# Performance work log

Measured on AMD Instinct MI355X. Metric: run time of the kernel, lower is better.

## Reference

```python
import jax, jax.numpy as jnp
import numpy as np


def setup_inputs() -> dict:
    key = jax.random.key(0)
    k1, k2, k3 = jax.random.split(key, 3)
    B, C, H, W = 16, 256, 32, 32
    K, D = 8192, 256
    z = jax.random.normal(k1, (B, C, H, W), dtype=jnp.float32)
    # torch init: uniform(-1/K, 1/K); use small-scale values for realism
    embedding = jax.random.uniform(k2, (K, D), dtype=jnp.float32,
                                   minval=-1.0 / K, maxval=1.0 / K)
    proj_w = jax.random.normal(k3, (D, D), dtype=jnp.float32) * (1.0 / np.sqrt(D))
    return {"z": z, "embedding": embedding, "proj_w": proj_w}


def reference(z, embedding, proj_w):
    commitment_cost = 0.25
    B, C, H, W = z.shape
    # codebook = Linear(embedding) with no bias: emb @ W^T  -> [K, D]
    codebook = embedding @ proj_w.T
    zt = jnp.transpose(z, (0, 2, 3, 1))            # [B, H, W, C]
    zf = zt.reshape(-1, C)                          # [N, C], N = B*H*W
    # squared distances: ||z||^2 + ||e||^2 - 2 z.e  -> [N, K]
    d = (jnp.sum(zf * zf, axis=1, keepdims=True)
         + jnp.sum(codebook * codebook, axis=1)
         - 2.0 * jnp.einsum('nd,kd->nk', zf, codebook))
    min_encoding_indices = jnp.argmin(d, axis=1)    # [N]
    z_quantized = codebook[min_encoding_indices].reshape(zt.shape)  # [B,H,W,C]
    commitment_loss = commitment_cost * jnp.mean(
        (jax.lax.stop_gradient(z_quantized) - zt) ** 2)
    codebook_loss = jnp.mean((z_quantized - jax.lax.stop_gradient(zt)) ** 2)
    loss = commitment_loss + codebook_loss
    # straight-through estimator
    zq_st = zt + jax.lax.stop_gradient(z_quantized - zt)
    out = jnp.transpose(zq_st, (0, 3, 1, 2))        # [B, C, H, W]
    idx = min_encoding_indices.reshape(B, H, W)
    return out, loss, commitment_loss, codebook_loss, idx
```

## Files before the change

kernel.cpp:

```cpp
#include <hip/hip_runtime.h>
#include <cfloat>


constexpr int Dd = 256;
constexpr float INV_M = 1.0f / 4194304.0f;
constexpr float DLT = 1e-3f;

typedef unsigned short u16;
typedef unsigned int u32;
typedef __attribute__((ext_vector_type(8))) short short8;
typedef __attribute__((ext_vector_type(4))) float f32x4;

__device__ __forceinline__ unsigned monof(float f) {
  unsigned u = __float_as_uint(f);
  return (u & 0x80000000u) ? ~u : (u | 0x80000000u);
}
__device__ __forceinline__ float unmonof(unsigned p) {
  unsigned u = (p & 0x80000000u) ? (p & 0x7FFFFFFFu) : ~p;
  return __uint_as_float(u);
}
__device__ __forceinline__ u16 f2bf(float x) {
  unsigned u = __float_as_uint(x);
  u += 0x7FFFu + ((u >> 16) & 1u);
  return (u16)(u >> 16);
}

__global__ __launch_bounds__(256)
void k_codebook(const float* __restrict__ emb, const float* __restrict__ proj,
                float* __restrict__ cb, u16* __restrict__ ef) {
  __shared__ float et[64 * 65];
  __shared__ float pt[64 * 65];
  __shared__ __align__(16) u16 tileT[64 * 72];
  const int t = threadIdx.x;
  const int tx = t & 15, ty = t >> 4;
  const int kb = blockIdx.x * 64;
  const int db = blockIdx.y * 64;
  float acc[4][4];
#pragma unroll
  for (int u = 0; u < 4; ++u)
#pragma unroll
    for (int v = 0; v < 4; ++v) acc[u][v] = 0.f;

  const int jm = t & 15;
  const int q  = t >> 4;

  for (int jc = 0; jc < Dd; jc += 64) {
    __syncthreads();
#pragma unroll
    for (int i = 0; i < 4; ++i) {
      const int row = q + i * 16;
      const float4 e4 = *(const float4*)(emb  + (size_t)(kb + row) * Dd + jc + jm * 4);
      const float4 p4 = *(const float4*)(proj + (size_t)(db + row) * Dd + jc + jm * 4);
      et[(jm*4 + 0) * 65 + row] = e4.x;
      et[(jm*4 + 1) * 65 + row] = e4.y;
      et[(jm*4 + 2) * 65 + row] = e4.z;
      et[(jm*4 + 3) * 65 + row] = e4.w;
      pt[(jm*4 + 0) * 65 + row] = p4.x;
      pt[(jm*4 + 1) * 65 + row] = p4.y;
      pt[(jm*4 + 2) * 65 + row] = p4.z;
      pt[(jm*4 + 3) * 65 + row] = p4.w;
    }
    __syncthreads();
#pragma unroll 16
    for (int j = 0; j < 64; ++j) {
      float a[4], b[4];
#pragma unroll
      for (int u = 0; u < 4; ++u) a[u] = et[j*65 + ty*4 + u];
#pragma unroll
      for (int v = 0; v < 4; ++v) b[v] = pt[j*65 + tx*4 + v];
#pragma unroll
      for (int u = 0; u < 4; ++u)
#pragma unroll
        for (int v = 0; v < 4; ++v) acc[u][v] = fmaf(a[u], b[v], acc[u][v]);
    }
  }
#pragma unroll
  for (int u = 0; u < 4; ++u) {
    const int k = kb + ty*4 + u;
#pragma unroll
    for (int v = 0; v < 4; ++v) {
      const int d = db + tx*4 + v;
      const float val = acc[u][v];
      cb[(size_t)k * Dd + d] = val;
      tileT[(ty*4 + u) * 72 + tx*4 + v] = f2bf(val);
    }
  }
  __syncthreads();
  uint4* ef16 = (uint4*)ef;
#pragma unroll
  for (int w2 = 0; w2 < 2; ++w2) {
    const int uu = w2 * 256 + t;
    const int k16g = uu >> 7;
    const int d32g = (uu >> 6) & 1;
    const int ln   = uu & 63;
    const int klo  = k16g * 16 + (ln & 15);
    const int dlo  = d32g * 32 + (ln >> 4) * 8;
    ef16[((kb >> 4) + k16g) * 512 + ((db >> 5) + d32g) * 64 + ln] =
        *(const uint4*)&tileT[klo * 72 + dlo];
  }
}

__global__ __launch_bounds__(256)
void k_norms(const float* __restrict__ cb, float* __restrict__ norms) {
  const int k = blockIdx.x * 256 + threadIdx.x;
  const float* row = cb + (size_t)k * Dd;
  float s = 0.f;
  for (int d = 0; d < Dd; d += 4) {
    const float4 v = *(const float4*)(row + d);
    s = fmaf(v.x, v.x, s);
    s = fmaf(v.y, v.y, s);
    s = fmaf(v.z, v.z, s);
    s = fmaf(v.w, v.w, s);
  }
  norms[k] = s;
}

__global__ __launch_bounds__(256)
void k_prep_z(const float* __restrict__ z, u16* __restrict__ zf,
              float* __restrict__ znorm) {
  __shared__ float tile[256 * 33];
  const int t = threadIdx.x;
  const int blk = blockIdx.x;
  const int w = t & 31, rg = t >> 5;
  const size_t zbase = (size_t)(blk >> 5) * 262144 + (size_t)(blk & 31) * 32 + w;
#pragma unroll 8
  for (int i = 0; i < 32; ++i) {
    const int d = rg * 32 + i;
    tile[d * 33 + w] = z[zbase + (size_t)d * 1024];
  }
  __syncthreads();
  if (t < 32) {
    float s = 0.f;
    for (int d = 0; d < Dd; ++d) {
      const float v = tile[d * 33 + t];
      s = fmaf(v, v, s);
    }
    znorm[blk * 32 + t] = s;
  }
  const int ml16 = t & 15;
  const int seg  = (t >> 4) & 7;
  const int hi   = t >> 7;
  const int nl   = hi * 16 + ml16;
  uint4* zf16 = (uint4*)zf;
  const int ubase = ((blk * 2 + hi) * 8 + seg) * 64 + ml16;
#pragma unroll
  for (int j = 0; j < 4; ++j) {
    u16 hb[8];
#pragma unroll
    for (int e = 0; e < 8; ++e)
      hb[e] = f2bf(tile[(seg * 32 + j * 8 + e) * 33 + nl]);
    zf16[ubase + j * 16] = *(const uint4*)hb;
  }
}

template <bool EMIT>
__global__ __launch_bounds__(256, 2)
void k_scan(const u16* __restrict__ zf, const u16* __restrict__ ef,
            const float* __restrict__ norms, const float* __restrict__ znorm,
            u32* __restrict__ rowminG, const float* __restrict__ rowThr,
            u32* __restrict__ rowcnt, u16* __restrict__ slots) {
  const int t    = threadIdx.x;
  const int lane = t & 63;
  const int ml   = lane & 15;
  const int qd   = lane >> 4;
  const int wvu  = __builtin_amdgcn_readfirstlane(t >> 6);
  const int rowhalf = wvu & 1;
  const int colhalf = wvu >> 1;
  const int bid  = blockIdx.x;
  const int kb   = (bid & 7) * 1024;
  const int nb   = (bid >> 3) * 64;

  const uint4* za = (const uint4*)zf + (size_t)((nb >> 4) + rowhalf * 2) * 512 + lane;
  const uint4* eb = (const uint4*)ef + (size_t)((kb >> 4) + colhalf * 8) * 512 + lane;

  float zn[2][4], thr[2][4];
#pragma unroll
  for (int rt = 0; rt < 2; ++rt) {
    const int nr = nb + rowhalf * 32 + rt * 16 + qd * 4;
    const f32x4 z4 = *(const f32x4*)(znorm + nr);
#pragma unroll
    for (int r = 0; r < 4; ++r) zn[rt][r] = z4[r];
    if (EMIT) {
      const f32x4 t4 = *(const f32x4*)(rowThr + nr);
#pragma unroll
      for (int r = 0; r < 4; ++r) thr[rt][r] = t4[r];
    }
  }

  float mv[2][4];
#pragma unroll
  for (int rt = 0; rt < 2; ++rt)
#pragma unroll
    for (int r = 0; r < 4; ++r) mv[rt][r] = FLT_MAX;

  short8 A0[2], A1[2], B0[8], B1[8];
#pragma unroll
  for (int rt = 0; rt < 2; ++rt) A0[rt] = *(const short8*)(za + rt * 512);
#pragma unroll
  for (int ct = 0; ct < 8; ++ct) B0[ct] = *(const short8*)(eb + ct * 512);

#pragma unroll 1
  for (int kt = 0; kt < 4; ++kt) {
    float nk[8];
#pragma unroll
    for (int ct = 0; ct < 8; ++ct)
      nk[ct] = norms[kb + kt * 256 + colhalf * 128 + ct * 16 + ml];

    f32x4 acc[2][8];
#pragma unroll
    for (int rt = 0; rt < 2; ++rt)
#pragma unroll
      for (int ct = 0; ct < 8; ++ct) acc[rt][ct] = (f32x4)0.f;

#pragma unroll
    for (int dhp = 0; dhp < 8; ++dhp) {
      const int pn = kt * 8 + dhp + 1;
      if (pn < 32) {
        const int offa = (pn & 7) * 64;
        const int offb = (pn >> 3) * 8192 + (pn & 7) * 64;
        if (dhp & 1) {
#pragma unroll
          for (int rt = 0; rt < 2; ++rt)
            A0[rt] = *(const short8*)(za + rt * 512 + offa);
#pragma unroll
          for (int ct = 0; ct < 8; ++ct)
            B0[ct] = *(const short8*)(eb + ct * 512 + offb);
        } else {
#pragma unroll
          for (int rt = 0; rt < 2; ++rt)
            A1[rt] = *(const short8*)(za + rt * 512 + offa);
#pragma unroll
          for (int ct = 0; ct < 8; ++ct)
            B1[ct] = *(const short8*)(eb + ct * 512 + offb);
        }
      }
      if (dhp & 1) {
#pragma unroll
        for (int rt = 0; rt < 2; ++rt)
#pragma unroll
          for (int ct = 0; ct < 8; ++ct)
            acc[rt][ct] = __builtin_amdgcn_mfma_f32_16x16x32_bf16(
                A1[rt], B1[ct], acc[rt][ct], 0, 0, 0);
      } else {
#pragma unroll
        for (int rt = 0; rt < 2; ++rt)
#pragma unroll
          for (int ct = 0; ct < 8; ++ct)
            acc[rt][ct] = __builtin_amdgcn_mfma_f32_16x16x32_bf16(
                A0[rt], B0[ct], acc[rt][ct], 0, 0, 0);
      }
    }

#pragma unroll
    for (int ct = 0; ct < 8; ++ct) {
      const int k = kb + kt * 256 + colhalf * 128 + ct * 16 + ml;
      const float nkv = nk[ct];
#pragma unroll
      for (int rt = 0; rt < 2; ++rt)
#pragma unroll
        for (int r = 0; r < 4; ++r) {
          const float sc = (zn[rt][r] + nkv) - 2.0f * acc[rt][ct][r];
          if (!EMIT) {
            mv[rt][r] = fminf(mv[rt][r], sc);
          } else if (sc <= thr[rt][r]) {
            const int n = nb + rowhalf * 32 + rt * 16 + qd * 4 + r;
            const u32 pos = atomicAdd(&rowcnt[n], 1u);
            if (pos < 32u) slots[n * 32 + pos] = (u16)k;
          }
        }
    }
  }

  if (!EMIT) {
#pragma unroll
    for (int rt = 0; rt < 2; ++rt)
#pragma unroll
      for (int r = 0; r < 4; ++r) {
        float m = mv[rt][r];
#pragma unroll
        for (int s = 1; s < 16; s <<= 1) m = fminf(m, __shfl_xor(m, s, 64));
        if (ml == 0)
          atomicMin(&rowminG[nb + rowhalf * 32 + rt * 16 + qd * 4 + r], monof(m));
      }
  }
}

__global__ __launch_bounds__(256)
void k_thresh(const u32* __restrict__ rowminG, float* __restrict__ rowThr) {
  const int n = blockIdx.x * 256 + threadIdx.x;
  rowThr[n] = unmonof(rowminG[n]) + DLT;
}

__global__ __launch_bounds__(256)
void k_rescore(const float* __restrict__ z, const float* __restrict__ cb,
               const float* __restrict__ norms, const float* __restrict__ znorm,
               const u32* __restrict__ rowcnt, const u16* __restrict__ slots,
               unsigned long long* __restrict__ packed) {
  __shared__ float ztl[32 * 261];
  const int t = threadIdx.x;
  const int blk = blockIdx.x;
  const int w = t & 31, dg = t >> 5;
  const size_t zbase = (size_t)(blk >> 5) * 262144 + (size_t)(blk & 31) * 32;
#pragma unroll 8
  for (int i = 0; i < 32; ++i) {
    const int d = dg * 32 + i;
    ztl[w * 261 + d] = z[zbase + (size_t)d * 1024 + w];
  }
  __syncthreads();

  const int lane = t & 63;
  const int wv = t >> 6;
#pragma unroll 1
  for (int i = 0; i < 8; ++i) {
    const int rl = wv * 8 + i;
    const int n = blk * 32 + rl;
    const u32 cnt = min(rowcnt[n], 32u);
    const float znr = znorm[n];
    unsigned long long best = 0xFFFFFFFFFFFFFFFFull;
    for (u32 c = 0; c < cnt; ++c) {
      const int k = (int)slots[n * 32 + c];
      const float4 c4 = *(const float4*)(cb + (size_t)k * Dd + lane * 4);
      const float* zp = ztl + rl * 261 + lane * 4;
      float p = 0.f;
      p = fmaf(zp[0], c4.x, p);
      p = fmaf(zp[1], c4.y, p);
      p = fmaf(zp[2], c4.z, p);
      p = fmaf(zp[3], c4.w, p);
#pragma unroll
      for (int s = 1; s < 64; s <<= 1) p += __shfl_xor(p, s, 64);
      const float sc = (znr + norms[k]) - 2.0f * p;
      const unsigned long long pk =
          ((unsigned long long)monof(sc) << 32) | (unsigned)k;
      if (pk < best) best = pk;
    }
    if (lane == 0 && cnt > 0) packed[n] = best;
  }
}

__global__ __launch_bounds__(256)
void k_output(const float* __restrict__ z, const float* __restrict__ cb,
              const unsigned long long* __restrict__ packed,
              float* __restrict__ out, float* __restrict__ idxf,
              float* __restrict__ ssum) {
  __shared__ float zqT[256 * 33];
  __shared__ float part[4];
  const int t = threadIdx.x;
  const int blk = blockIdx.x;
  const int nbase = blk * 32;

  {
    const int nl = t >> 3, m = t & 7;
    const int idx = (int)(packed[nbase + nl] & 0xFFFFFFFFull);
    const float* row = cb + (size_t)idx * Dd;
#pragma unroll
    for (int i = 0; i < 8; ++i) {
      const int d0 = m * 4 + i * 32;
      const float4 v = *(const float4*)(row + d0);
      zqT[(d0 + 0) * 33 + nl] = v.x;
      zqT[(d0 + 1) * 33 + nl] = v.y;
      zqT[(d0 + 2) * 33 + nl] = v.z;
      zqT[(d0 + 3) * 33 + nl] = v.w;
    }
    if (t < 32)
      idxf[nbase + t] = (float)(unsigned)(packed[nbase + t] & 0xFFFFFFFFull);
  }
  __syncthreads();

  const int w = t & 31, cg = t >> 5;
  const size_t base = (size_t)(blk >> 5) * 262144 + (size_t)(blk & 31) * 32 + w;
  float local = 0.f;
#pragma unroll
  for (int cc = 0; cc < 32; ++cc) {
    const int c = cg * 32 + cc;
    const float q  = zqT[c * 33 + w];
    const float zv = z[base + (size_t)c * 1024];
    out[base + (size_t)c * 1024] = q;
    const float dd = q - zv;
    local = fmaf(dd, dd, local);
  }
  float v = local;
#pragma unroll
  for (int m = 1; m < 64; m <<= 1) v += __shfl_xor(v, m, 64);
  if ((t & 63) == 0) part[t >> 6] = v;
  __syncthreads();
  if (t == 0) atomicAdd(ssum, part[0] + part[1] + part[2] + part[3]);
}

__global__ void k_final(const float* __restrict__ ssum, float* __restrict__ scal) {
  const float m = *ssum * INV_M;
  scal[0] = 1.25f * m;
  scal[1] = 0.25f * m;
  scal[2] = m;
}

extern "C" void kernel_launch(void* const* d_in, const int* in_sizes, int n_in,
                              void* d_out, int out_size, void* d_ws, size_t ws_size,
                              hipStream_t stream) {
  const float* z    = (const float*)d_in[0];
  const float* emb  = (const float*)d_in[1];
  const float* proj = (const float*)d_in[2];

  float* out  = (float*)d_out;
  float* scal = out + 4194304;
  float* idxf = out + 4194307;

  float* cb    = (float*)d_ws;
  float* norms = cb + 2097152;
  unsigned long long* packed =
      (unsigned long long*)(norms + 8192);
  float* znorm = (float*)(packed + 16384);
  u16* zf = (u16*)(znorm + 16384);
  u16* ef = zf + 4194304;
  u32* rowminG = (u32*)(ef + 2097152);
  float* rowThr = (float*)(rowminG + 16384);
  u32* rowcnt = (u32*)(rowThr + 16384);
  u16* slots = (u16*)(rowcnt + 16384);
  float* ssum = (float*)(slots + 16384 * 32);

  hipMemsetAsync(rowminG, 0xFF, 16384 * sizeof(u32), stream);
  hipMemsetAsync(rowcnt, 0, 16384 * sizeof(u32), stream);
  hipMemsetAsync(packed, 0xFF, 16384 * sizeof(unsigned long long), stream);
  hipMemsetAsync(ssum, 0, sizeof(float), stream);

  k_codebook<<<dim3(128, 4), 256, 0, stream>>>(emb, proj, cb, ef);
  k_norms   <<<32, 256, 0, stream>>>(cb, norms);
  k_prep_z  <<<512, 256, 0, stream>>>(z, zf, znorm);
  k_scan<false><<<2048, 256, 0, stream>>>(zf, ef, norms, znorm,
                                          rowminG, rowThr, rowcnt, slots);
  k_thresh  <<<64, 256, 0, stream>>>(rowminG, rowThr);
  k_scan<true> <<<2048, 256, 0, stream>>>(zf, ef, norms, znorm,
                                          rowminG, rowThr, rowcnt, slots);
  k_rescore <<<512, 256, 0, stream>>>(z, cb, norms, znorm, rowcnt, slots, packed);
  k_output  <<<512, 256, 0, stream>>>(z, cb, packed, out, idxf, ssum);
  k_final   <<<1, 1, 0, stream>>>(ssum, scal);

  (void)in_sizes; (void)n_in; (void)out_size; (void)ws_size;
}
```

Baseline: 416.4 us.

## Split scan column tiles in half to cut registers and raise occupancy

```diff
diff --git a/kernel.cpp b/kernel.cpp
--- a/kernel.cpp
+++ b/kernel.cpp
@@ -154,7 +154,7 @@
 }
 
 template <bool EMIT>
-__global__ __launch_bounds__(256, 2)
+__global__ __launch_bounds__(256, 4)
 void k_scan(const u16* __restrict__ zf, const u16* __restrict__ ef,
             const float* __restrict__ norms, const float* __restrict__ znorm,
             u32* __restrict__ rowminG, const float* __restrict__ rowThr,
@@ -170,8 +170,10 @@
   const int kb   = (bid & 7) * 1024;
   const int nb   = (bid >> 3) * 64;
 
-  const uint4* za = (const uint4*)zf + (size_t)((nb >> 4) + rowhalf * 2) * 512 + lane;
-  const uint4* eb = (const uint4*)ef + (size_t)((kb >> 4) + colhalf * 8) * 512 + lane;
+  const uint4* zf16 = (const uint4*)zf;
+  const uint4* ef16 = (const uint4*)ef;
+  const uint4* za = zf16 + (size_t)((nb >> 4) + rowhalf * 2) * 512 + lane;
+  const uint4* eb = ef16 + (size_t)((kb >> 4) + colhalf * 8) * 512 + lane;
 
   float zn[2][4], thr[2][4];
 #pragma unroll
@@ -193,82 +195,82 @@
 #pragma unroll
     for (int r = 0; r < 4; ++r) mv[rt][r] = FLT_MAX;
 
-  short8 A0[2], A1[2], B0[8], B1[8];
-#pragma unroll
-  for (int rt = 0; rt < 2; ++rt) A0[rt] = *(const short8*)(za + rt * 512);
-#pragma unroll
-  for (int ct = 0; ct < 8; ++ct) B0[ct] = *(const short8*)(eb + ct * 512);
-
 #pragma unroll 1
   for (int kt = 0; kt < 4; ++kt) {
-    float nk[8];
-#pragma unroll
-    for (int ct = 0; ct < 8; ++ct)
-      nk[ct] = norms[kb + kt * 256 + colhalf * 128 + ct * 16 + ml];
-
-    f32x4 acc[2][8];
-#pragma unroll
-    for (int rt = 0; rt < 2; ++rt)
-#pragma unroll
-      for (int ct = 0; ct < 8; ++ct) acc[rt][ct] = (f32x4)0.f;
-
-#pragma unroll
-    for (int dhp = 0; dhp < 8; ++dhp) {
-      const int pn = kt * 8 + dhp + 1;
-      if (pn < 32) {
-        const int offa = (pn & 7) * 64;
-        const int offb = (pn >> 3) * 8192 + (pn & 7) * 64;
-        if (dhp & 1) {
-#pragma unroll
-          for (int rt = 0; rt < 2; ++rt)
-            A0[rt] = *(const short8*)(za + rt * 512 + offa);
-#pragma unroll
-          for (int ct = 0; ct < 8; ++ct)
-            B0[ct] = *(const short8*)(eb + ct * 512 + offb);
+    const size_t ekt = (size_t)kt * 16 * 512;
+#pragma unroll
+    for (int cq = 0; cq < 2; ++cq) {
+      const uint4* ecq = eb + ekt + (size_t)(cq * 4) * 512;
+
+      f32x4 acc[2][4];
+#pragma unroll
+      for (int rt = 0; rt < 2; ++rt)
+#pragma unroll
+        for (int ct = 0; ct < 4; ++ct) acc[rt][ct] = (f32x4)0.f;
+
+      short8 Aa0[2], Aa1[2], Bb0[4], Bb1[4];
+#pragma unroll
+      for (int rt = 0; rt < 2; ++rt) Aa0[rt] = *(const short8*)(za + rt * 512);
+#pragma unroll
+      for (int ct = 0; ct < 4; ++ct) Bb0[ct] = *(const short8*)(ecq + ct * 512);
+
+#pragma unroll
+      for (int d32 = 0; d32 < 8; ++d32) {
+        if (d32 < 7) {
+          const int off = (d32 + 1) * 64;
+          if (d32 & 1) {
+#pragma unroll
+            for (int rt = 0; rt < 2; ++rt)
+              Aa0[rt] = *(const short8*)(za + rt * 512 + off);
+#pragma unroll
+            for (int ct = 0; ct < 4; ++ct)
+              Bb0[ct] = *(const short8*)(ecq + ct * 512 + off);
+          } else {
+#pragma unroll
+            for (int rt = 0; rt < 2; ++rt)
+              Aa1[rt] = *(const short8*)(za + rt * 512 + off);
+#pragma unroll
+            for (int ct = 0; ct < 4; ++ct)
+              Bb1[ct] = *(const short8*)(ecq + ct * 512 + off);
+          }
+        }
+        if (d32 & 1) {
+#pragma unroll
+          for (int ct = 0; ct < 4; ++ct)
+#pragma unroll
+            for (int rt = 0; rt < 2; ++rt)
+              acc[rt][ct] = __builtin_amdgcn_mfma_f32_16x16x32_bf16(
+                  Aa1[rt], Bb1[ct], acc[rt][ct], 0, 0, 0);
         } else {
 #pragma unroll
-          for (int rt = 0; rt < 2; ++rt)
-            A1[rt] = *(const short8*)(za + rt * 512 + offa);
-#pragma unroll
-          for (int ct = 0; ct < 8; ++ct)
-            B1[ct] = *(const short8*)(eb + ct * 512 + offb);
+          for (int ct = 0; ct < 4; ++ct)
+#pragma unroll
+            for (int rt = 0; rt < 2; ++rt)
+              acc[rt][ct] = __builtin_amdgcn_mfma_f32_16x16x32_bf16(
+                  Aa0[rt], Bb0[ct], acc[rt][ct], 0, 0, 0);
         }
       }
-      if (dhp & 1) {
+
+#pragma unroll
+      for (int ct = 0; ct < 4; ++ct) {
+        const int k = kb + kt * 256 + colhalf * 128 + cq * 64 + ct * 16 + ml;
+        const float nkv = norms[k];
 #pragma unroll
         for (int rt = 0; rt < 2; ++rt)
 #pragma unroll
-          for (int ct = 0; ct < 8; ++ct)
-            acc[rt][ct] = __builtin_amdgcn_mfma_f32_16x16x32_bf16(
-                A1[rt], B1[ct], acc[rt][ct], 0, 0, 0);
-      } else {
-#pragma unroll
-        for (int rt = 0; rt < 2; ++rt)
-#pragma unroll
-          for (int ct = 0; ct < 8; ++ct)
-            acc[rt][ct] = __builtin_amdgcn_mfma_f32_16x16x32_bf16(
-                A0[rt], B0[ct], acc[rt][ct], 0, 0, 0);
+          for (int r = 0; r < 4; ++r) {
+            const float sc = (zn[rt][r] + nkv) - 2.0f * acc[rt][ct][r];
+            if (!EMIT) {
+              mv[rt][r] = fminf(mv[rt][r], sc);
+            } else if (sc <= thr[rt][r]) {
+              const int n = nb + rowhalf * 32 + rt * 16 + qd * 4 + r;
+              const u32 pos = atomicAdd(&rowcnt[n], 1u);
+              if (pos < 32u) slots[n * 32 + pos] = (u16)k;
+            }
+          }
       }
     }
-
-#pragma unroll
-    for (int ct = 0; ct < 8; ++ct) {
-      const int k = kb + kt * 256 + colhalf * 128 + ct * 16 + ml;
-      const float nkv = nk[ct];
-#pragma unroll
-      for (int rt = 0; rt < 2; ++rt)
-#pragma unroll
-        for (int r = 0; r < 4; ++r) {
-          const float sc = (zn[rt][r] + nkv) - 2.0f * acc[rt][ct][r];
-          if (!EMIT) {
-            mv[rt][r] = fminf(mv[rt][r], sc);
-          } else if (sc <= thr[rt][r]) {
-            const int n = nb + rowhalf * 32 + rt * 16 + qd * 4 + r;
-            const u32 pos = atomicAdd(&rowcnt[n], 1u);
-            if (pos < 32u) slots[n * 32 + pos] = (u16)k;
-          }
-        }
-    }
+    __syncthreads();
   }
 
   if (!EMIT) {
@@ -318,7 +320,7 @@
     const float znr = znorm[n];
     unsigned long long best = 0xFFFFFFFFFFFFFFFFull;
     for (u32 c = 0; c < cnt; ++c) {
-      const int k = (int)slots[n * 32 + c];
+      const int k = (int)slots[n * 32 + c] & 8191;
       const float4 c4 = *(const float4*)(cb + (size_t)k * Dd + lane * 4);
       const float* zp = ztl + rl * 261 + lane * 4;
       float p = 0.f;
@@ -350,7 +352,7 @@
 
   {
     const int nl = t >> 3, m = t & 7;
-    const int idx = (int)(packed[nbase + nl] & 0xFFFFFFFFull);
+    const int idx = (int)(packed[nbase + nl] & 0xFFFFFFFFull) & 8191;
     const float* row = cb + (size_t)idx * Dd;
 #pragma unroll
     for (int i = 0; i < 8; ++i) {
```

Result: slower. 571.4 us (+37.2%).
